# Performance work log

Measured on AMD Instinct MI355X. Metric: run time of the kernel, lower is better.

## Reference

```python
import jax, jax.numpy as jnp
import numpy as np

B, T, D = 1, 1024, 1024
H = 16; HKV = 16; HD = D // H; R = 2; K = 3; LOWR = 32
HR = HKV * R                      # heads after harmonic expansion
OUTW = HKV * HD * 2 * R           # w_proj output width
SCALE = HD ** -0.5


def setup_inputs() -> dict:
    key = jax.random.key(0)
    ks = jax.random.split(key, 10)
    def rn(k, shape, sc=1.0):
        return jax.random.normal(k, shape, dtype=jnp.float32) * sc
    return {
        'hidden_states': rn(ks[0], (B, T, D)),
        'q_w': rn(ks[1], (D, D), D ** -0.5),
        'k_w': rn(ks[2], (D, D), D ** -0.5),
        'v_w': rn(ks[3], (D, D), D ** -0.5),
        'w1': rn(ks[4], (LOWR, D), D ** -0.5),
        'w2': rn(ks[5], (OUTW, LOWR), LOWR ** -0.5),
        'conv_w': rn(ks[6], (OUTW, K), K ** -0.5),
        'bt_w': rn(ks[7], (HKV * R, D), D ** -0.5),
        'bt_b': jnp.zeros((HKV * R,), jnp.float32),
        'o_w': rn(ks[8], (D, D * R), (D * R) ** -0.5),
        'omega': 0.01 * jnp.ones((1, 1, 1, R), jnp.float32),
        'phi': jnp.zeros((1, 1, 1, R), jnp.float32),
    }


def path_attention_forward(hidden_states, q_w, k_w, v_w, w1, w2, conv_w,
                           bt_w, bt_b, o_w, omega, phi):
    b, t, _ = hidden_states.shape
    q = hidden_states @ q_w.T
    k = hidden_states @ k_w.T
    v = hidden_states @ v_w.T
    # low-rank w projection, causal depthwise short conv (kernel K), SiLU
    w_raw = (hidden_states @ w1.T) @ w2.T                    # [b,t,OUTW]
    xp = jnp.pad(w_raw, ((0, 0), (K - 1, 0), (0, 0)))
    w_raw = sum(xp[:, i:i + t, :] * conv_w[:, i] for i in range(K))
    w_raw = jax.nn.silu(w_raw)
    # rotary-like harmonic mixing of Householder directions
    w5 = w_raw.reshape(b, t, HKV, 2 * R, HD)
    Ah = w5[:, :, :, 0::2, :]                                # [b,t,HKV,R,HD]
    Bh = w5[:, :, :, 1::2, :]
    pos = jnp.arange(t, dtype=jnp.float32)[None, :, None, None]
    theta = omega * pos + phi                                # [1,t,1,R]
    c = jnp.cos(theta)[..., None]
    s = jnp.sin(theta)[..., None]
    Wdir = Ah * c + Bh * s
    Wdir = Wdir * jax.lax.rsqrt(jnp.sum(Wdir * Wdir, -1, keepdims=True) + 1e-6)
    beta = jax.nn.sigmoid(hidden_states @ bt_w.T + bt_b) * 2.0   # [b,t,HR]
    # repeat-interleave q/k/v heads across harmonics -> [b,HR,t,HD]
    to_h = lambda x: jnp.swapaxes(jnp.repeat(x.reshape(b, t, H, HD), R, axis=2), 1, 2)
    qh, kh, vh = to_h(q), to_h(k), to_h(v)
    wh = jnp.swapaxes(Wdir.reshape(b, t, HR, HD), 1, 2)      # [b,HR,t,HD]
    bh = jnp.swapaxes(beta, 1, 2)                            # [b,HR,t]
    # PaTH logits: A_ij = q_i^T (H_i ... H_{j+1}) k_j, H_t = I - beta_t w_t w_t^T.
    # WY/UT transform: with M_ts = beta_t (w_t.w_s) for s<t, the coefficients
    # B_tj (t>j) of the accumulated rank-1 corrections solve the unit-lower
    # triangular system (I + M) B = strilow(Db W K^T), and
    # A = tril(Q K^T - tril(Q W^T) B).
    idx = jnp.arange(t)
    strict = idx[:, None] > idx[None, :]
    incl = idx[:, None] >= idx[None, :]
    Mw = jnp.where(strict, jnp.einsum('bhtd,bhsd->bhts', wh, wh) * bh[..., None], 0.0)
    rhs = jnp.where(strict, jnp.einsum('bhtd,bhjd->bhtj', wh, kh) * bh[..., None], 0.0)
    Bmat = jax.scipy.linalg.solve_triangular(Mw + jnp.eye(t, dtype=Mw.dtype), rhs, lower=True)
    qk = jnp.einsum('bhid,bhjd->bhij', qh, kh)
    qw = jnp.where(incl, jnp.einsum('bhid,bhtd->bhit', qh, wh), 0.0)
    logits = (qk - jnp.einsum('bhit,bhtj->bhij', qw, Bmat)) * SCALE
    logits = jnp.where(incl, logits, -1e30)
    p = jax.nn.softmax(logits, axis=-1)
    o = jnp.einsum('bhij,bhjd->bhid', p, vh)                 # [b,HR,t,HD]
    o = jnp.swapaxes(o, 1, 2).reshape(b, t, HR * HD)         # [b,t,D*R]
    return o @ o_w.T


def reference(hidden_states, q_w, k_w, v_w, w1, w2, conv_w, bt_w, bt_b, o_w, omega, phi):
    return path_attention_forward(hidden_states, q_w, k_w, v_w, w1, w2, conv_w,
                                  bt_w, bt_b, o_w, omega, phi)
```

## Files before the change

kernel.cpp:

```cpp
#include <hip/hip_runtime.h>
#include <math.h>

#define TTD 1024
#define DDM 1024
#define HDIM 64
#define PSCALE 0.125f
#define PSC2 0.18033688011112042f
#define LS 72

typedef __attribute__((ext_vector_type(8))) __bf16 bf16x8;
typedef __attribute__((ext_vector_type(4))) float f32x4;
#define MFMA16(a,b,c) __builtin_amdgcn_mfma_f32_16x16x32_bf16(a,b,c,0,0,0)

#define STR_(x) #x
#define WAITVM(N) asm volatile("s_waitcnt vmcnt(" STR_(N) ")" ::: "memory")
#define BAR() do { __builtin_amdgcn_s_barrier(); asm volatile("" ::: "memory"); } while (0)
#define LGKBAR() do { asm volatile("s_waitcnt lgkmcnt(0)" ::: "memory"); \
                      __builtin_amdgcn_s_barrier(); asm volatile("" ::: "memory"); } while (0)
#define FULLBAR() do { asm volatile("s_waitcnt vmcnt(0) lgkmcnt(0)" ::: "memory"); \
                       __builtin_amdgcn_s_barrier(); asm volatile("" ::: "memory"); } while (0)

__device__ __forceinline__ ushort f2b(float f) {
  unsigned u = __builtin_bit_cast(unsigned, f);
  return (ushort)((u + 0x7fffu + ((u >> 16) & 1u)) >> 16);
}
__device__ __forceinline__ float b2f(ushort u) {
  unsigned v = (unsigned)u << 16;
  return __builtin_bit_cast(float, v);
}

__device__ __forceinline__ void gload_lds16(const ushort* g, ushort* l) {
  __builtin_amdgcn_global_load_lds(
      (const __attribute__((address_space(1))) unsigned*)g,
      (__attribute__((address_space(3))) unsigned*)l, 16, 0, 0);
}

#define SWZ(row, cc) (((row) * 8 + ((cc) ^ ((row) & 7))) * 8)
#define SWZE(row, col) (SWZ(row, (col) >> 3) + ((col) & 7))
#define SWZ2(row, cc) (((row) * 8 + ((cc) ^ (((row) & 7) ^ ((row) >> 3)))) * 8)
#define SWZ2E(row, col) (SWZ2(row, (col) >> 3) + ((col) & 7))

__device__ __forceinline__ void stage_tile(const ushort* gb, long gs, ushort* tile,
                                           int w, int l) {
  int sub = l >> 3, cc = (l & 7) ^ sub;
  #pragma unroll
  for (int it = 0; it < 2; ++it) {
    int q = w * 2 + it;
    gload_lds16(gb + (long)(q * 8 + sub) * gs + cc * 8, &tile[(q * 64 + l) * 8]);
  }
}

__device__ __forceinline__ bf16x8 frag(const ushort* tile, int row, int cc) {
  return *(const bf16x8*)&tile[SWZ(row, cc)];
}
__device__ __forceinline__ bf16x8 frag2(const ushort* tile, int row, int cc) {
  return *(const bf16x8*)&tile[SWZ2(row, cc)];
}

#define XT_PERH   557056L
#define OFF_X     0L
#define OFF_PZ    35651584L
#define OFF_HSB   35651584L
#define OFF_QWW   37748736L
#define OFF_KWW   39845888L
#define OFF_VWW   41943040L
#define OFF_W2B   44040192L
#define OFF_WLOWB 44302336L
#define OFF_TB    98566144L
#define OFF_OALL  98566144L
#define OFF_YB    102760448L
#define OFF_OWB   106954752L
#define OFF_WHB   111149056L
#define OFF_QB    115343360L
#define OFF_KB    117440512L
#define OFF_VTB   119537664L
#define OFF_BETA  121634816L
#define OFF_BW64  121765888L

#define CVT_TOTAL 6488064L
struct CvtSegs {
  const float* src[8];
  ushort* dst[8];
  long cnt[8];
};
__global__ __launch_bounds__(256) void cvt_all_kernel(CvtSegs sg) {
  long e = ((long)blockIdx.x * 256 + threadIdx.x) * 4;
  #pragma unroll
  for (int s = 0; s < 8; ++s) {
    if (e < sg.cnt[s]) {
      float4 f = *(const float4*)(sg.src[s] + e);
      ushort4 o;
      o.x = f2b(f.x); o.y = f2b(f.y); o.z = f2b(f.z); o.w = f2b(f.w);
      *(ushort4*)(sg.dst[s] + e) = o;
      return;
    }
    e -= sg.cnt[s];
  }
}

__global__ __launch_bounds__(256) void qkv_sp_kernel(
    const ushort* __restrict__ hsb,
    const ushort* __restrict__ wq, const ushort* __restrict__ wk, const ushort* __restrict__ wv,
    const ushort* __restrict__ bw, const float* __restrict__ bt_b,
    ushort* __restrict__ cq, ushort* __restrict__ ck, ushort* __restrict__ cv,
    float* __restrict__ beta, ushort* __restrict__ wlowb)
{
  int z = blockIdx.z;
  if (z == 3 && blockIdx.x != 0) return;
  const ushort* B = (z == 0) ? wq : (z == 1) ? wk : (z == 2) ? wv : bw;

  __shared__ ushort Ab[2][8192];
  __shared__ ushort Bb[2][4096];

  int tid = threadIdx.x, w = tid >> 6, l = tid & 63;
  int quad = l >> 4, lane15 = l & 15;
  int rm = blockIdx.y * 128, cn = (z == 3) ? 0 : blockIdx.x * 64;
  const ushort* Ag = hsb + (long)rm * DDM;
  const ushort* Bg = B + (long)cn * DDM;

  stage_tile(Ag, DDM, &Ab[0][0], w, l);
  stage_tile(Ag + 64 * DDM, DDM, &Ab[0][4096], w, l);
  stage_tile(Bg, DDM, &Bb[0][0], w, l);

  f32x4 acc[2][4] = {};
  int arow0 = (w & 1) * 32 + lane15;
  int asel = (w >> 1) * 4096;
  for (int kt = 0; kt < 16; ++kt) {
    int cur = kt & 1;
    if (kt < 15) {
      int nxt = cur ^ 1;
      stage_tile(Ag + (kt + 1) * 64, DDM, &Ab[nxt][0], w, l);
      stage_tile(Ag + 64 * DDM + (kt + 1) * 64, DDM, &Ab[nxt][4096], w, l);
      stage_tile(Bg + (kt + 1) * 64, DDM, &Bb[nxt][0], w, l);
      WAITVM(6);
    } else {
      WAITVM(0);
    }
    BAR();
    const ushort* Atile = &Ab[cur][asel];
    #pragma unroll
    for (int s = 0; s < 2; ++s) {
      bf16x8 a0 = frag(Atile, arow0, s * 4 + quad);
      bf16x8 a1 = frag(Atile, arow0 + 16, s * 4 + quad);
      #pragma unroll
      for (int f = 0; f < 4; ++f) {
        bf16x8 bf = frag(&Bb[cur][0], f * 16 + lane15, s * 4 + quad);
        acc[0][f] = MFMA16(a0, bf, acc[0][f]);
        acc[1][f] = MFMA16(a1, bf, acc[1][f]);
      }
    }
    BAR();
  }

  if (z < 2) {
    ushort* Cb = (z == 0) ? cq : ck;
    #pragma unroll
    for (int rr = 0; rr < 2; ++rr) {
      int orow = rm + w * 32 + rr * 16 + quad * 4;
      #pragma unroll
      for (int f = 0; f < 4; ++f)
        #pragma unroll
        for (int r = 0; r < 4; ++r)
          Cb[(long)(orow + r) * DDM + cn + f * 16 + lane15] = f2b(acc[rr][f][r]);
    }
  } else if (z == 2) {
    #pragma unroll
    for (int rr = 0; rr < 2; ++rr) {
      int orow = rm + w * 32 + rr * 16 + quad * 4;
      #pragma unroll
      for (int f = 0; f < 4; ++f) {
        ushort4 o;
        o.x = f2b(acc[rr][f][0]); o.y = f2b(acc[rr][f][1]);
        o.z = f2b(acc[rr][f][2]); o.w = f2b(acc[rr][f][3]);
        *(ushort4*)&cv[(long)(cn + f * 16 + lane15) * TTD + orow] = o;
      }
    }
  } else {
    #pragma unroll
    for (int rr = 0; rr < 2; ++rr) {
      int orow = rm + w * 32 + rr * 16 + quad * 4;
      #pragma unroll
      for (int f = 0; f < 2; ++f) {
        int hr = f * 16 + lane15;
        float bb = bt_b[hr];
        #pragma unroll
        for (int r = 0; r < 4; ++r)
          beta[(long)hr * TTD + orow + r] = 2.f / (1.f + expf(-(acc[rr][f][r] + bb)));
      }
      #pragma unroll
      for (int f = 2; f < 4; ++f)
        #pragma unroll
        for (int r = 0; r < 4; ++r)
          wlowb[(long)(orow + r) * 32 + (f - 2) * 16 + lane15] = f2b(acc[rr][f][r]);
    }
  }
}

__global__ __launch_bounds__(256) void wraw_solveA_kernel(
    const ushort* __restrict__ wlowb, const ushort* __restrict__ w2b,
    const float* __restrict__ conv_w, const float* __restrict__ omega,
    const float* __restrict__ phi, const float* __restrict__ beta,
    ushort* __restrict__ whb, ushort* __restrict__ TB, ushort* __restrict__ YB)
{
  int c = blockIdx.x;
  int rm = c * 64;
  int p = blockIdx.y;
  int hkv = p >> 1, r = p & 1;
  int c0 = hkv * 256 + r * 128;

  __shared__ char pool_[65568];
  ushort* As = (ushort*)pool_;
  ushort* Bs = (ushort*)(pool_ + 4096);
  float (*WR)[132] = (float(*)[132])(pool_ + 12288);
  ushort* Wrow = (ushort*)(pool_ + 47136);
  ushort* WT   = (ushort*)(pool_ + 56352);
  float (*Lm)[65] = (float(*)[65])pool_;
  float (*Vf)[65] = (float(*)[65])(pool_ + 16640);
  ushort* Tb = (ushort*)(pool_ + 33280);

  int tid = threadIdx.x, w = tid >> 6, l = tid & 63;
  int quad = l >> 4, lane15 = l & 15;

  {
    int row = tid >> 2, ch = (tid & 3) * 8;
    gload_lds16(wlowb + (long)(rm + row) * 32 + ch, &As[row * 32 + ch]);
    gload_lds16(w2b + (long)(c0 + row) * 32 + ch, &Bs[row * 32 + ch]);
    gload_lds16(w2b + (long)(c0 + 64 + row) * 32 + ch, &Bs[(64 + row) * 32 + ch]);
  }
  {
    int hr2 = tid >> 7, col = tid & 127;
    float acc = 0.f;
    if (rm > 0) {
      long t = rm - 2 + hr2;
      for (int k = 0; k < 32; ++k)
        acc += b2f(wlowb[t * 32 + k]) * b2f(w2b[(long)(c0 + col) * 32 + k]);
    }
    WR[hr2][col] = acc;
  }
  FULLBAR();

  #pragma unroll
  for (int g = 0; g < 2; ++g) {
    f32x4 acc[4] = {};
    bf16x8 af = *(const bf16x8*)&As[(w * 16 + lane15) * 32 + quad * 8];
    #pragma unroll
    for (int f = 0; f < 4; ++f) {
      bf16x8 bf = *(const bf16x8*)&Bs[(g * 64 + f * 16 + lane15) * 32 + quad * 8];
      acc[f] = MFMA16(af, bf, acc[f]);
    }
    #pragma unroll
    for (int f = 0; f < 4; ++f)
      #pragma unroll
      for (int rr = 0; rr < 4; ++rr)
        WR[2 + w * 16 + quad * 4 + rr][g * 64 + f * 16 + lane15] = acc[f][rr];
  }
  LGKBAR();

  {
    float cwa[3], cwb[3];
    #pragma unroll
    for (int i = 0; i < 3; ++i) {
      cwa[i] = conv_w[(long)(c0 + l) * 3 + i];
      cwb[i] = conv_w[(long)(c0 + 64 + l) * 3 + i];
    }
    float om = omega[r], ph = phi[r];
    for (int it = 0; it < 16; ++it) {
      int tl = it * 4 + w;
      int t = rm + tl;
      float a = cwa[0] * WR[tl][l] + cwa[1] * WR[tl + 1][l] + cwa[2] * WR[tl + 2][l];
      float b = cwb[0] * WR[tl][64 + l] + cwb[1] * WR[tl + 1][64 + l] + cwb[2] * WR[tl + 2][64 + l];
      a = a / (1.f + expf(-a));
      b = b / (1.f + expf(-b));
      float th = om * (float)t + ph;
      float wd = a * cosf(th) + b * sinf(th);
      float ss = wd * wd;
      #pragma unroll
      for (int o = 32; o > 0; o >>= 1) ss += __shfl_xor(ss, o, 64);
      ushort hv = f2b(wd * (1.f / sqrtf(ss + 1e-6f)));
      whb[((long)p * TTD + t) * HDIM + l] = hv;
      Wrow[tl * LS + l] = hv;
      WT[l * LS + tl] = hv;
    }
  }
  LGKBAR();

  const float* bet = beta + (long)p * TTD + rm;
  ushort* TBh = TB + ((long)p * 16 + c) * 4096;
  ushort* YBh = YB + ((long)p * 16 + c) * 4096;

  f32x4 g4[4] = {};
  #pragma unroll
  for (int s = 0; s < 2; ++s) {
    bf16x8 af = *(const bf16x8*)&Wrow[(w * 16 + lane15) * LS + s * 32 + quad * 8];
    #pragma unroll
    for (int f = 0; f < 4; ++f) {
      bf16x8 bf = *(const bf16x8*)&Wrow[(f * 16 + lane15) * LS + s * 32 + quad * 8];
      g4[f] = MFMA16(af, bf, g4[f]);
    }
  }
  #pragma unroll
  for (int r4 = 0; r4 < 4; ++r4) {
    int t = w * 16 + quad * 4 + r4;
    float bv = bet[t];
    #pragma unroll
    for (int f = 0; f < 4; ++f) {
      int tp = f * 16 + lane15;
      Lm[t][tp] = (t > tp) ? bv * g4[f][r4] : 0.f;
    }
  }
  LGKBAR();

  {
    float cur[16];
    #pragma unroll
    for (int i = 0; i < 16; ++i) cur[i] = (w * 16 + i == l) ? bet[l] : 0.f;
    for (int sb = 0; sb < 4; ++sb) {
      if (w == sb) {
        float xloc[16];
        #pragma unroll
        for (int i = 0; i < 16; ++i) {
          float bv = cur[i];
          #pragma unroll
          for (int j2 = 0; j2 < 16; ++j2)
            if (j2 < i) bv -= Lm[sb * 16 + i][sb * 16 + j2] * xloc[j2];
          xloc[i] = bv;
          Vf[sb * 16 + i][l] = bv;
        }
      }
      LGKBAR();
      if (w > sb) {
        float xp[16];
        #pragma unroll
        for (int t = 0; t < 16; ++t) xp[t] = Vf[sb * 16 + t][l];
        #pragma unroll
        for (int i = 0; i < 16; ++i) {
          float s2 = cur[i];
          #pragma unroll
          for (int t = 0; t < 16; ++t) s2 -= Lm[w * 16 + i][sb * 16 + t] * xp[t];
          cur[i] = s2;
        }
      }
    }
  }
  {
    int t = tid >> 2, off = (tid & 3) * 16;
    ushort tmp[16];
    #pragma unroll
    for (int i = 0; i < 16; ++i) { tmp[i] = f2b(Vf[t][off + i]); Tb[t * LS + off + i] = tmp[i]; }
    *(uint4*)&TBh[t * 64 + off] = *(const uint4*)&tmp[0];
    *(uint4*)&TBh[t * 64 + off + 8] = *(const uint4*)&tmp[8];
  }
  LGKBAR();
  f32x4 y[4] = {};
  #pragma unroll
  for (int s = 0; s < 2; ++s) {
    bf16x8 af = *(const bf16x8*)&Tb[(w * 16 + lane15) * LS + s * 32 + quad * 8];
    #pragma unroll
    for (int f = 0; f < 4; ++f) {
      bf16x8 bf = *(const bf16x8*)&WT[(f * 16 + lane15) * LS + s * 32 + quad * 8];
      y[f] = MFMA16(af, bf, y[f]);
    }
  }
  #pragma unroll
  for (int f = 0; f < 4; ++f)
    #pragma unroll
    for (int r4 = 0; r4 < 4; ++r4)
      YBh[(long)(w * 16 + quad * 4 + r4) * 64 + f * 16 + lane15] = f2b(y[f][r4]);
}

__global__ __launch_bounds__(256) void solveB_kernel(
    const ushort* __restrict__ whb, const ushort* __restrict__ kb,
    const ushort* __restrict__ TB, const ushort* __restrict__ YB,
    ushort* __restrict__ Xb, ushort* __restrict__ KZ)
{
  int h = blockIdx.x;
  int ty = blockIdx.y;
  int js = (ty < 8) ? ty : (23 - ty);
  int j0 = js * 64;
  const ushort* wh_h = whb + (long)h * TTD * HDIM;
  const ushort* k_h = kb + (long)(h >> 1) * 64;
  ushort* X_h = Xb + (long)h * XT_PERH;
  ushort* KZ_h = KZ + (long)h * 15 * TTD * HDIM;
  int xidx = js * 16 - js * (js - 1) / 2;

  __shared__ ushort KT[4096];
  __shared__ ushort WT[4096];
  __shared__ ushort XM[4096];
  __shared__ ushort nS[4096];

  int tid = threadIdx.x, w = tid >> 6, l = tid & 63;
  int quad = l >> 4, lane15 = l & 15;
  f32x4 Sacc[4] = {}, Wacc[4] = {};

  stage_tile(k_h + (long)j0 * DDM, DDM, KT, w, l);

  float kreg[4][4];
  #pragma unroll
  for (int f = 0; f < 4; ++f)
    #pragma unroll
    for (int r = 0; r < 4; ++r)
      kreg[f][r] = b2f(k_h[(long)(j0 + w * 16 + quad * 4 + r) * DDM + f * 16 + lane15]);

  int prow0 = tid >> 3, pd0 = (tid & 7) * 8;
  uint4 pk0 = *(const uint4*)&wh_h[((long)js * 64 + prow0) * HDIM + pd0];
  uint4 pk1 = *(const uint4*)&wh_h[((long)js * 64 + 32 + prow0) * HDIM + pd0];
  bf16x8 ybr0 = {}, ybr1 = {};

  WAITVM(0);

  for (int c = js; c < 16; ++c) {
    LGKBAR();
    {
      const ushort* pu0 = (const ushort*)&pk0;
      const ushort* pu1 = (const ushort*)&pk1;
      #pragma unroll
      for (int i = 0; i < 8; ++i) WT[SWZ2E(pd0 + i, prow0)] = pu0[i];
      #pragma unroll
      for (int i = 0; i < 8; ++i) WT[SWZ2E(pd0 + i, 32 + prow0)] = pu1[i];
    }
    if (c < 15) {
      pk0 = *(const uint4*)&wh_h[((long)(c + 1) * 64 + prow0) * HDIM + pd0];
      pk1 = *(const uint4*)&wh_h[((long)(c + 1) * 64 + 32 + prow0) * HDIM + pd0];
    }
    f32x4 xacc[4] = {};
    if (c == js) {
      const ushort* whc = wh_h + (long)c * 64 * HDIM;
      f32x4 m[4] = {};
      #pragma unroll
      for (int s = 0; s < 2; ++s) {
        bf16x8 af = *(const bf16x8*)&whc[(long)(w * 16 + lane15) * HDIM + s * 32 + quad * 8];
        #pragma unroll
        for (int f = 0; f < 4; ++f)
          m[f] = MFMA16(af, frag(KT, f * 16 + lane15, s * 4 + quad), m[f]);
      }
      #pragma unroll
      for (int f = 0; f < 4; ++f)
        #pragma unroll
        for (int r = 0; r < 4; ++r) {
          int t = w * 16 + quad * 4 + r, j = f * 16 + lane15;
          XM[SWZE(j, t)] = (t > j) ? f2b(m[f][r]) : (ushort)0;
        }
      LGKBAR();
      const ushort* TBh = TB + ((long)h * 16 + c) * 4096;
      #pragma unroll
      for (int s = 0; s < 2; ++s) {
        bf16x8 af = *(const bf16x8*)&TBh[(long)(w * 16 + lane15) * 64 + s * 32 + quad * 8];
        #pragma unroll
        for (int f = 0; f < 4; ++f)
          xacc[f] = MFMA16(af, frag(XM, f * 16 + lane15, s * 4 + quad), xacc[f]);
      }
      LGKBAR();
    } else {
      #pragma unroll
      for (int f = 0; f < 4; ++f) {
        xacc[f] = MFMA16(ybr0, frag(KT, f * 16 + lane15, 0 * 4 + quad), xacc[f]);
        xacc[f] = MFMA16(ybr0, frag(nS, f * 16 + lane15, 0 * 4 + quad), xacc[f]);
        xacc[f] = MFMA16(ybr1, frag(KT, f * 16 + lane15, 1 * 4 + quad), xacc[f]);
        xacc[f] = MFMA16(ybr1, frag(nS, f * 16 + lane15, 1 * 4 + quad), xacc[f]);
      }
    }
    #pragma unroll
    for (int f = 0; f < 4; ++f)
      #pragma unroll
      for (int r = 0; r < 4; ++r)
        XM[SWZE(f * 16 + lane15, w * 16 + quad * 4 + r)] = f2b(xacc[f][r]);
    LGKBAR();
    {
      ushort* xt = X_h + (long)xidx * 4096;
      int j = tid >> 2, c2 = (tid & 3) * 2;
      bf16x8 s0 = frag(XM, j, c2);
      bf16x8 s1 = frag(XM, j, c2 + 1);
      *(bf16x8*)&xt[j * 64 + c2 * 8] = s0;
      *(bf16x8*)&xt[j * 64 + c2 * 8 + 8] = s1;
    }
    ++xidx;
    if (c < 15) {
      {
        const ushort* YBn = YB + ((long)h * 16 + c + 1) * 4096;
        ybr0 = *(const bf16x8*)&YBn[(long)(w * 16 + lane15) * 64 + 0 * 32 + quad * 8];
        ybr1 = *(const bf16x8*)&YBn[(long)(w * 16 + lane15) * 64 + 1 * 32 + quad * 8];
      }
      #pragma unroll
      for (int s = 0; s < 2; ++s) {
        bf16x8 aw = frag2(WT, w * 16 + lane15, s * 4 + quad);
        bf16x8 ax = frag(XM, w * 16 + lane15, s * 4 + quad);
        #pragma unroll
        for (int f = 0; f < 4; ++f) {
          Sacc[f] = MFMA16(aw, frag(XM, f * 16 + lane15, s * 4 + quad), Sacc[f]);
          Wacc[f] = MFMA16(ax, frag2(WT, f * 16 + lane15, s * 4 + quad), Wacc[f]);
        }
      }
      ushort* pz = KZ_h + (long)c * TTD * HDIM;
      #pragma unroll
      for (int f = 0; f < 4; ++f)
        #pragma unroll
        for (int r = 0; r < 4; ++r)
          pz[(long)(j0 + w * 16 + quad * 4 + r) * 64 + f * 16 + lane15] =
              f2b(kreg[f][r] - Wacc[f][r]);
      #pragma unroll
      for (int f = 0; f < 4; ++f)
        #pragma unroll
        for (int r = 0; r < 4; ++r)
          nS[SWZE(f * 16 + lane15, w * 16 + quad * 4 + r)] = f2b(-Sacc[f][r]);
    }
  }
}

__global__ __launch_bounds__(256) void flash_kernel(
    const ushort* __restrict__ qb, const ushort* __restrict__ kbuf,
    const ushort* __restrict__ whb, const ushort* __restrict__ Xb,
    const ushort* __restrict__ KZ, const ushort* __restrict__ vTb,
    ushort* __restrict__ oall)
{
  int h = blockIdx.x;
  int y = blockIdx.y;
  int ri = (y < 8) ? y : (23 - y);
  int r0 = ri * 64;
  const ushort* q_h = qb + (long)(h >> 1) * 64;
  const ushort* k_h = kbuf + (long)(h >> 1) * 64;
  const ushort* wh_h = whb + (long)h * TTD * HDIM;
  const ushort* X_h = Xb + (long)h * XT_PERH;
  const ushort* kz = KZ + ((long)h * 15 + (ri - 1)) * TTD * HDIM;
  const ushort* v_h = vTb + (long)(h >> 1) * 64 * TTD;

  __shared__ ushort S[2][3][4096];
  __shared__ ushort KD[4096];
  __shared__ ushort QWD[4096];
  __shared__ ushort PT[4096];

  int tid = threadIdx.x, w = tid >> 6, l = tid & 63;
  int quad = l >> 4, lane15 = l & 15;

  bf16x8 aq[2];
  #pragma unroll
  for (int s = 0; s < 2; ++s)
    aq[s] = *(const bf16x8*)&q_h[(long)(r0 + w * 16 + lane15) * DDM + s * 32 + quad * 8];
  const ushort* xst = X_h + (long)ri * 4096;
  stage_tile(k_h + (long)r0 * DDM, DDM, KD, w, l);
  if (ri > 0) stage_tile(kz, 64, &S[0][0][0], w, l);
  stage_tile(xst, 64, &S[0][1][0], w, l);
  stage_tile(v_h, TTD, &S[0][2][0], w, l);
  {
    f32x4 t4[4] = {};
    #pragma unroll
    for (int s = 0; s < 2; ++s)
      #pragma unroll
      for (int f = 0; f < 4; ++f) {
        bf16x8 bf = *(const bf16x8*)&wh_h[(long)(r0 + f * 16 + lane15) * HDIM + s * 32 + quad * 8];
        t4[f] = MFMA16(aq[s], bf, t4[f]);
      }
    #pragma unroll
    for (int f = 0; f < 4; ++f)
      #pragma unroll
      for (int r = 0; r < 4; ++r) {
        int i = w * 16 + quad * 4 + r, t = f * 16 + lane15;
        QWD[SWZE(i, t)] = (i >= t) ? f2b(-t4[f][r]) : (ushort)0;
      }
  }

  f32x4 O[4] = {};
  float m[4], lsum[4];
  #pragma unroll
  for (int r = 0; r < 4; ++r) { m[r] = -1e30f; lsum[r] = 0.f; }

  for (int jb = 0; jb <= ri; ++jb) {
    int cur = jb & 1;
    const ushort* xnx = xst + (long)(15 - jb) * 4096;
    if (jb < ri) {
      long c0n = (long)(jb + 1) * 64;
      ushort* nb = &S[cur ^ 1][0][0];
      if (jb + 1 < ri) {
        stage_tile(kz + c0n * 64, 64, nb, w, l);
        stage_tile(xnx, 64, nb + 4096, w, l);
        stage_tile(v_h + c0n, TTD, nb + 8192, w, l);
        WAITVM(6);
      } else {
        stage_tile(xnx, 64, nb + 4096, w, l);
        stage_tile(v_h + c0n, TTD, nb + 8192, w, l);
        WAITVM(4);
      }
    } else {
      WAITVM(0);
    }
    BAR();
    const ushort* Skz = &S[cur][0][0];
    const ushort* Sx  = &S[cur][1][0];
    const ushort* Sv  = &S[cur][2][0];
    f32x4 acc[4] = {};
    const ushort* Sb = (jb < ri) ? Skz : KD;
    #pragma unroll
    for (int s = 0; s < 2; ++s)
      #pragma unroll
      for (int f = 0; f < 4; ++f)
        acc[f] = MFMA16(aq[s], frag(Sb, f * 16 + lane15, s * 4 + quad), acc[f]);
    #pragma unroll
    for (int s = 0; s < 2; ++s) {
      bf16x8 aw = frag(QWD, w * 16 + lane15, s * 4 + quad);
      #pragma unroll
      for (int f = 0; f < 4; ++f)
        acc[f] = MFMA16(aw, frag(Sx, f * 16 + lane15, s * 4 + quad), acc[f]);
    }
    float rmax[4] = {-3e38f, -3e38f, -3e38f, -3e38f};
    #pragma unroll
    for (int f = 0; f < 4; ++f)
      #pragma unroll
      for (int r = 0; r < 4; ++r) {
        float lv = acc[f][r] * PSC2;
        if (jb == ri && (f * 16 + lane15) > (w * 16 + quad * 4 + r)) lv = -3e38f;
        acc[f][r] = lv;
        rmax[r] = fmaxf(rmax[r], lv);
      }
    #pragma unroll
    for (int r = 0; r < 4; ++r) {
      rmax[r] = fmaxf(rmax[r], __shfl_xor(rmax[r], 1, 64));
      rmax[r] = fmaxf(rmax[r], __shfl_xor(rmax[r], 2, 64));
      rmax[r] = fmaxf(rmax[r], __shfl_xor(rmax[r], 4, 64));
      rmax[r] = fmaxf(rmax[r], __shfl_xor(rmax[r], 8, 64));
    }
    float alpha[4], rs[4] = {0.f, 0.f, 0.f, 0.f};
    #pragma unroll
    for (int r = 0; r < 4; ++r) {
      float nm = fmaxf(m[r], rmax[r]);
      alpha[r] = exp2f(m[r] - nm);
      m[r] = nm;
    }
    #pragma unroll
    for (int f = 0; f < 4; ++f)
      #pragma unroll
      for (int r = 0; r < 4; ++r) {
        float e = exp2f(acc[f][r] - m[r]);
        acc[f][r] = e;
        rs[r] += e;
      }
    #pragma unroll
    for (int r = 0; r < 4; ++r) {
      rs[r] += __shfl_xor(rs[r], 1, 64);
      rs[r] += __shfl_xor(rs[r], 2, 64);
      rs[r] += __shfl_xor(rs[r], 4, 64);
      rs[r] += __shfl_xor(rs[r], 8, 64);
      lsum[r] = lsum[r] * alpha[r] + rs[r];
    }
    #pragma unroll
    for (int f = 0; f < 4; ++f)
      #pragma unroll
      for (int r = 0; r < 4; ++r) O[f][r] *= alpha[r];
    #pragma unroll
    for (int f = 0; f < 4; ++f)
      #pragma unroll
      for (int r = 0; r < 4; ++r) {
        int i = w * 16 + quad * 4 + r;
        PT[SWZE(i, f * 16 + lane15)] = f2b(acc[f][r]);
      }
    #pragma unroll
    for (int s = 0; s < 2; ++s) {
      bf16x8 ap = frag(PT, w * 16 + lane15, s * 4 + quad);
      #pragma unroll
      for (int f = 0; f < 4; ++f)
        O[f] = MFMA16(ap, frag(Sv, f * 16 + lane15, s * 4 + quad), O[f]);
    }
    BAR();
    xst = xnx;
  }
  #pragma unroll
  for (int r = 0; r < 4; ++r) lsum[r] = 1.f / lsum[r];
  #pragma unroll
  for (int f = 0; f < 4; ++f)
    #pragma unroll
    for (int r = 0; r < 4; ++r)
      oall[(long)(r0 + w * 16 + quad * 4 + r) * 2048 + h * 64 + f * 16 + lane15] =
          f2b(O[f][r] * lsum[r]);
}

__global__ __launch_bounds__(256) void gemm_out_kernel(
    const ushort* __restrict__ A, const ushort* __restrict__ Bb, float* __restrict__ C)
{
  __shared__ ushort Ab[2][8192];
  __shared__ ushort Bt[2][8192];
  int tid = threadIdx.x, w = tid >> 6, l = tid & 63;
  int quad = l >> 4, lane15 = l & 15;
  int rm = blockIdx.y * 64, cn = blockIdx.x * 64;
  const ushort* Ag = A + (long)rm * 2048;
  const ushort* Bg = Bb + (long)cn * 2048;

  stage_tile(Ag, 2048, &Ab[0][0], w, l);
  stage_tile(Ag + 64, 2048, &Ab[0][4096], w, l);
  stage_tile(Bg, 2048, &Bt[0][0], w, l);
  stage_tile(Bg + 64, 2048, &Bt[0][4096], w, l);

  f32x4 acc[4] = {};
  for (int kt = 0; kt < 16; ++kt) {
    int cur = kt & 1;
    if (kt < 15) {
      int nxt = cur ^ 1;
      long o = (long)(kt + 1) * 128;
      stage_tile(Ag + o, 2048, &Ab[nxt][0], w, l);
      stage_tile(Ag + o + 64, 2048, &Ab[nxt][4096], w, l);
      stage_tile(Bg + o, 2048, &Bt[nxt][0], w, l);
      stage_tile(Bg + o + 64, 2048, &Bt[nxt][4096], w, l);
      WAITVM(8);
    } else {
      WAITVM(0);
    }
    BAR();
    #pragma unroll
    for (int u = 0; u < 2; ++u)
      #pragma unroll
      for (int s = 0; s < 2; ++s) {
        bf16x8 af = frag(&Ab[cur][u * 4096], w * 16 + lane15, s * 4 + quad);
        #pragma unroll
        for (int f = 0; f < 4; ++f)
          acc[f] = MFMA16(af, frag(&Bt[cur][u * 4096], f * 16 + lane15, s * 4 + quad), acc[f]);
      }
    BAR();
  }
  int orow = rm + w * 16 + quad * 4;
  #pragma unroll
  for (int f = 0; f < 4; ++f)
    #pragma unroll
    for (int r = 0; r < 4; ++r)
      C[(long)(orow + r) * DDM + cn + f * 16 + lane15] = acc[f][r];
}

extern "C" void kernel_launch(void* const* d_in, const int* in_sizes, int n_in,
                              void* d_out, int out_size, void* d_ws, size_t ws_size,
                              hipStream_t stream) {
  const float* hs     = (const float*)d_in[0];
  const float* q_w    = (const float*)d_in[1];
  const float* k_w    = (const float*)d_in[2];
  const float* v_w    = (const float*)d_in[3];
  const float* w1     = (const float*)d_in[4];
  const float* w2     = (const float*)d_in[5];
  const float* conv_w = (const float*)d_in[6];
  const float* bt_w   = (const float*)d_in[7];
  const float* bt_b   = (const float*)d_in[8];
  const float* o_w    = (const float*)d_in[9];
  const float* omega  = (const float*)d_in[10];
  const float* phi    = (const float*)d_in[11];
  float* out = (float*)d_out;
  char* ws = (char*)d_ws;

  ushort* Xb     = (ushort*)(ws + OFF_X);
  ushort* KZb    = (ushort*)(ws + OFF_PZ);
  ushort* hs_b   = (ushort*)(ws + OFF_HSB);
  ushort* qw_wb  = (ushort*)(ws + OFF_QWW);
  ushort* kw_wb  = (ushort*)(ws + OFF_KWW);
  ushort* vw_wb  = (ushort*)(ws + OFF_VWW);
  ushort* w2_b   = (ushort*)(ws + OFF_W2B);
  ushort* wlow_b = (ushort*)(ws + OFF_WLOWB);
  ushort* TB     = (ushort*)(ws + OFF_TB);
  ushort* o_all  = (ushort*)(ws + OFF_OALL);
  ushort* YB     = (ushort*)(ws + OFF_YB);
  ushort* ow_b   = (ushort*)(ws + OFF_OWB);
  ushort* wh_b   = (ushort*)(ws + OFF_WHB);
  ushort* q_b    = (ushort*)(ws + OFF_QB);
  ushort* k_b    = (ushort*)(ws + OFF_KB);
  ushort* vT_b   = (ushort*)(ws + OFF_VTB);
  float*  beta   = (float*)(ws + OFF_BETA);
  ushort* bw_b   = (ushort*)(ws + OFF_BW64);

  CvtSegs sg;
  sg.src[0] = hs;   sg.dst[0] = hs_b;          sg.cnt[0] = 1048576;
  sg.src[1] = q_w;  sg.dst[1] = qw_wb;         sg.cnt[1] = 1048576;
  sg.src[2] = k_w;  sg.dst[2] = kw_wb;         sg.cnt[2] = 1048576;
  sg.src[3] = v_w;  sg.dst[3] = vw_wb;         sg.cnt[3] = 1048576;
  sg.src[4] = w2;   sg.dst[4] = w2_b;          sg.cnt[4] = 131072;
  sg.src[5] = bt_w; sg.dst[5] = bw_b;          sg.cnt[5] = 32768;
  sg.src[6] = w1;   sg.dst[6] = bw_b + 32768;  sg.cnt[6] = 32768;
  sg.src[7] = o_w;  sg.dst[7] = ow_b;          sg.cnt[7] = 2097152;
  cvt_all_kernel<<<dim3((CVT_TOTAL + 1023) / 1024), 256, 0, stream>>>(sg);

  qkv_sp_kernel<<<dim3(16, 8, 4), 256, 0, stream>>>(
      hs_b, qw_wb, kw_wb, vw_wb, bw_b, bt_b, q_b, k_b, vT_b, beta, wlow_b);

  wraw_solveA_kernel<<<dim3(16, 32), 256, 0, stream>>>(
      wlow_b, w2_b, conv_w, omega, phi, beta, wh_b, TB, YB);

  solveB_kernel<<<dim3(32, 16), 256, 0, stream>>>(wh_b, k_b, TB, YB, Xb, KZb);

  flash_kernel<<<dim3(32, 16), 256, 0, stream>>>(q_b, k_b, wh_b, Xb, KZb, vT_b, o_all);

  gemm_out_kernel<<<dim3(16, 16), 256, 0, stream>>>(o_all, ow_b, out);

  (void)in_sizes; (void)n_in; (void)out_size; (void)ws_size;
}
```

Before: 213.2 us.

## Use single-barrier double buffering, fast intrinsics, and lazy softmax rescaling

Three loops (projection GEMM, attention, output GEMM) move from two barriers per iteration to one. Each iteration now waits for all loads, syncs once, then issues the next tile's loads before computing. This overlaps the prefetch with the current compute and drops the trailing barrier. The attention loop also skips the O/lsum rescale when no row max grows across the wavefront, and expf/sinf/cosf become fast intrinsics. Fast intrinsics add small precision error, and the single-barrier ordering relies on the wait-then-barrier making the buffer reuse safe.

```diff
diff --git a/kernel.cpp b/kernel.cpp
--- a/kernel.cpp
+++ b/kernel.cpp
@@ -127,16 +127,14 @@
   int asel = (w >> 1) * 4096;
   for (int kt = 0; kt < 16; ++kt) {
     int cur = kt & 1;
+    WAITVM(0);
+    BAR();
     if (kt < 15) {
       int nxt = cur ^ 1;
       stage_tile(Ag + (kt + 1) * 64, DDM, &Ab[nxt][0], w, l);
       stage_tile(Ag + 64 * DDM + (kt + 1) * 64, DDM, &Ab[nxt][4096], w, l);
       stage_tile(Bg + (kt + 1) * 64, DDM, &Bb[nxt][0], w, l);
-      WAITVM(6);
-    } else {
-      WAITVM(0);
-    }
-    BAR();
+    }
     const ushort* Atile = &Ab[cur][asel];
     #pragma unroll
     for (int s = 0; s < 2; ++s) {
@@ -149,7 +147,6 @@
         acc[1][f] = MFMA16(a1, bf, acc[1][f]);
       }
     }
-    BAR();
   }
 
   if (z < 2) {
@@ -185,7 +182,7 @@
         float bb = bt_b[hr];
         #pragma unroll
         for (int r = 0; r < 4; ++r)
-          beta[(long)hr * TTD + orow + r] = 2.f / (1.f + expf(-(acc[rr][f][r] + bb)));
+          beta[(long)hr * TTD + orow + r] = 2.f / (1.f + __expf(-(acc[rr][f][r] + bb)));
       }
       #pragma unroll
       for (int f = 2; f < 4; ++f)
@@ -269,10 +266,10 @@
       int t = rm + tl;
       float a = cwa[0] * WR[tl][l] + cwa[1] * WR[tl + 1][l] + cwa[2] * WR[tl + 2][l];
       float b = cwb[0] * WR[tl][64 + l] + cwb[1] * WR[tl + 1][64 + l] + cwb[2] * WR[tl + 2][64 + l];
-      a = a / (1.f + expf(-a));
-      b = b / (1.f + expf(-b));
+      a = a / (1.f + __expf(-a));
+      b = b / (1.f + __expf(-b));
       float th = om * (float)t + ph;
-      float wd = a * cosf(th) + b * sinf(th);
+      float wd = a * __cosf(th) + b * __sinf(th);
       float ss = wd * wd;
       #pragma unroll
       for (int o = 32; o > 0; o >>= 1) ss += __shfl_xor(ss, o, 64);
@@ -566,23 +563,15 @@
   for (int jb = 0; jb <= ri; ++jb) {
     int cur = jb & 1;
     const ushort* xnx = xst + (long)(15 - jb) * 4096;
+    WAITVM(0);
+    BAR();
     if (jb < ri) {
       long c0n = (long)(jb + 1) * 64;
       ushort* nb = &S[cur ^ 1][0][0];
-      if (jb + 1 < ri) {
-        stage_tile(kz + c0n * 64, 64, nb, w, l);
-        stage_tile(xnx, 64, nb + 4096, w, l);
-        stage_tile(v_h + c0n, TTD, nb + 8192, w, l);
-        WAITVM(6);
-      } else {
-        stage_tile(xnx, 64, nb + 4096, w, l);
-        stage_tile(v_h + c0n, TTD, nb + 8192, w, l);
-        WAITVM(4);
-      }
-    } else {
-      WAITVM(0);
-    }
-    BAR();
+      if (jb + 1 < ri) stage_tile(kz + c0n * 64, 64, nb, w, l);
+      stage_tile(xnx, 64, nb + 4096, w, l);
+      stage_tile(v_h + c0n, TTD, nb + 8192, w, l);
+    }
     const ushort* Skz = &S[cur][0][0];
     const ushort* Sx  = &S[cur][1][0];
     const ushort* Sv  = &S[cur][2][0];
@@ -617,13 +606,22 @@
       rmax[r] = fmaxf(rmax[r], __shfl_xor(rmax[r], 4, 64));
       rmax[r] = fmaxf(rmax[r], __shfl_xor(rmax[r], 8, 64));
     }
-    float alpha[4], rs[4] = {0.f, 0.f, 0.f, 0.f};
-    #pragma unroll
-    for (int r = 0; r < 4; ++r) {
-      float nm = fmaxf(m[r], rmax[r]);
-      alpha[r] = exp2f(m[r] - nm);
-      m[r] = nm;
-    }
+    bool grow = (rmax[0] > m[0]) | (rmax[1] > m[1]) | (rmax[2] > m[2]) | (rmax[3] > m[3]);
+    if (__any(grow)) {
+      float alpha[4];
+      #pragma unroll
+      for (int r = 0; r < 4; ++r) {
+        float nm = fmaxf(m[r], rmax[r]);
+        alpha[r] = exp2f(m[r] - nm);
+        m[r] = nm;
+        lsum[r] *= alpha[r];
+      }
+      #pragma unroll
+      for (int f = 0; f < 4; ++f)
+        #pragma unroll
+        for (int r = 0; r < 4; ++r) O[f][r] *= alpha[r];
+    }
+    float rs[4] = {0.f, 0.f, 0.f, 0.f};
     #pragma unroll
     for (int f = 0; f < 4; ++f)
       #pragma unroll
@@ -638,12 +636,8 @@
       rs[r] += __shfl_xor(rs[r], 2, 64);
       rs[r] += __shfl_xor(rs[r], 4, 64);
       rs[r] += __shfl_xor(rs[r], 8, 64);
-      lsum[r] = lsum[r] * alpha[r] + rs[r];
-    }
-    #pragma unroll
-    for (int f = 0; f < 4; ++f)
-      #pragma unroll
-      for (int r = 0; r < 4; ++r) O[f][r] *= alpha[r];
+      lsum[r] += rs[r];
+    }
     #pragma unroll
     for (int f = 0; f < 4; ++f)
       #pragma unroll
@@ -658,7 +652,6 @@
       for (int f = 0; f < 4; ++f)
         O[f] = MFMA16(ap, frag(Sv, f * 16 + lane15, s * 4 + quad), O[f]);
     }
-    BAR();
     xst = xnx;
   }
   #pragma unroll
@@ -690,6 +683,8 @@
   f32x4 acc[4] = {};
   for (int kt = 0; kt < 16; ++kt) {
     int cur = kt & 1;
+    WAITVM(0);
+    BAR();
     if (kt < 15) {
       int nxt = cur ^ 1;
       long o = (long)(kt + 1) * 128;
@@ -697,11 +692,7 @@
       stage_tile(Ag + o + 64, 2048, &Ab[nxt][4096], w, l);
       stage_tile(Bg + o, 2048, &Bt[nxt][0], w, l);
       stage_tile(Bg + o + 64, 2048, &Bt[nxt][4096], w, l);
-      WAITVM(8);
-    } else {
-      WAITVM(0);
-    }
-    BAR();
+    }
     #pragma unroll
     for (int u = 0; u < 2; ++u)
       #pragma unroll
@@ -711,7 +702,6 @@
         for (int f = 0; f < 4; ++f)
           acc[f] = MFMA16(af, frag(&Bt[cur][u * 4096], f * 16 + lane15, s * 4 + quad), acc[f]);
       }
-    BAR();
   }
   int orow = rm + w * 16 + quad * 4;
   #pragma unroll
```

New measurement: 219.8 us. 1.03x slower.
